# Kernel optimization log

Measured on AMD Instinct MI355X. Metric: run time of the kernel, lower is better.

## Reference

```python
import jax, jax.numpy as jnp
import numpy as np

N = 100000
NEG_SLOPE = 0.2
ALPHA = 0.5


def _glorot(key, shape):
    fan_in, fan_out = shape[0], shape[-1]
    lim = jnp.sqrt(6.0 / (fan_in + fan_out))
    return jax.random.uniform(key, shape, jnp.float32, -lim, lim)


def setup_inputs() -> dict:
    key = jax.random.key(0)
    ks = jax.random.split(key, 16)
    x = jax.random.normal(ks[0], (N, 512), jnp.float32)
    spatial_edge_index = jax.random.randint(ks[1], (2, 800000), 0, N, jnp.int64)
    gene_sim_edge_index = jax.random.randint(ks[2], (2, 800000), 0, N, jnp.int64)
    # spatial GAT params (in=512 -> hid=256)
    W_sp = _glorot(ks[3], (512, 256)); a_src_sp = _glorot(ks[4], (256,)); a_dst_sp = _glorot(ks[5], (256,)); b_sp = jnp.zeros((256,), jnp.float32)
    # gene-sim GAT params
    W_gs = _glorot(ks[6], (512, 256)); a_src_gs = _glorot(ks[7], (256,)); a_dst_gs = _glorot(ks[8], (256,)); b_gs = jnp.zeros((256,), jnp.float32)
    # fusion GAT params (hid=256 -> out=64)
    W_fu = _glorot(ks[9], (256, 64)); a_src_fu = _glorot(ks[10], (64,)); a_dst_fu = _glorot(ks[11], (64,)); b_fu = jnp.zeros((64,), jnp.float32)
    return {"x": x, "spatial_edge_index": spatial_edge_index, "gene_sim_edge_index": gene_sim_edge_index,
            "W_sp": W_sp, "a_src_sp": a_src_sp, "a_dst_sp": a_dst_sp, "b_sp": b_sp,
            "W_gs": W_gs, "a_src_gs": a_src_gs, "a_dst_gs": a_dst_gs, "b_gs": b_gs,
            "W_fu": W_fu, "a_src_fu": a_src_fu, "a_dst_fu": a_dst_fu, "b_fu": b_fu}


def gat_conv(x, edge_index, W, a_src, a_dst, bias):
    """PyG GATConv, heads=1, concat=False, add_self_loops=True."""
    n = x.shape[0]
    h = x @ W  # [N, H]
    loops = jnp.arange(n, dtype=edge_index.dtype)
    src = jnp.concatenate([edge_index[0], loops])  # message source j
    dst = jnp.concatenate([edge_index[1], loops])  # aggregation target i
    e = jax.nn.leaky_relu((h @ a_src)[src] + (h @ a_dst)[dst], NEG_SLOPE)  # [E+N]
    # segment softmax over incoming edges of each dst node
    m = jax.ops.segment_max(e, dst, num_segments=n)
    ex = jnp.exp(e - m[dst])
    denom = jax.ops.segment_sum(ex, dst, num_segments=n)
    coef = ex / denom[dst]
    out = jax.ops.segment_sum(coef[:, None] * h[src], dst, num_segments=n)
    return out + bias


def reference(x, spatial_edge_index, gene_sim_edge_index,
              W_sp, a_src_sp, a_dst_sp, b_sp,
              W_gs, a_src_gs, a_dst_gs, b_gs,
              W_fu, a_src_fu, a_dst_fu, b_fu):
    h_spatial = jax.nn.elu(gat_conv(x, spatial_edge_index, W_sp, a_src_sp, a_dst_sp, b_sp))
    h_gene = jax.nn.elu(gat_conv(x, gene_sim_edge_index, W_gs, a_src_gs, a_dst_gs, b_gs))
    h_fused = ALPHA * h_gene + (1.0 - ALPHA) * h_spatial
    return gat_conv(h_fused, spatial_edge_index, W_fu, a_src_fu, a_dst_fu, b_fu)
```

## Files before the change

kernel.cpp:

```cpp
#include <hip/hip_runtime.h>
#include <math.h>


#define NEG_SLOPE 0.2f

typedef __attribute__((ext_vector_type(8))) short bf16x8;
typedef __attribute__((ext_vector_type(4))) float f32x4;

__device__ __forceinline__ unsigned short f2bf(float f) {
  unsigned int u = __float_as_uint(f);
  u = (u + 0x7FFFu + ((u >> 16) & 1u)) >> 16;
  return (unsigned short)u;
}
__device__ __forceinline__ float bf2f(unsigned short u) {
  return __uint_as_float((unsigned int)u << 16);
}
__device__ __forceinline__ int rl_i(int v, int l) {
  return __builtin_amdgcn_readlane(v, l);
}
__device__ __forceinline__ float rl_f(float v, int l) {
  return __uint_as_float(__builtin_amdgcn_readlane(__float_as_uint(v), l));
}

#define GLOAD16(g, l)                                                   \
  __builtin_amdgcn_global_load_lds(                                     \
      (const __attribute__((address_space(1))) void*)(g),               \
      (__attribute__((address_space(3))) void*)(l), 16, 0, 0)

__global__ __launch_bounds__(256) void wt_bf16_all(const float* __restrict__ W_sp,
                                                   const float* __restrict__ W_gs,
                                                   const float* __restrict__ W_fu,
                                                   unsigned short* __restrict__ wt_sp,
                                                   unsigned short* __restrict__ wt_gs,
                                                   unsigned short* __restrict__ wt_fu) {
  const int i = blockIdx.x * 256 + threadIdx.x;
  if (i < 131072) {
    const int k = i >> 8, n = i & 255;
    wt_sp[n * 512 + k] = f2bf(W_sp[i]);
  } else if (i < 262144) {
    const int j = i - 131072;
    const int k = j >> 8, n = j & 255;
    wt_gs[n * 512 + k] = f2bf(W_gs[j]);
  } else if (i < 278528) {
    const int j = i - 262144;
    const int k = j >> 6, n = j & 63;
    wt_fu[n * 256 + k] = f2bf(W_fu[j]);
  }
}

__global__ __launch_bounds__(256) void hist2(const int* __restrict__ dst_sp,
                                             const int* __restrict__ dst_gs,
                                             int* __restrict__ deg_sp,
                                             int* __restrict__ deg_gs, int E) {
  const int m = blockIdx.x * 256 + threadIdx.x;
  if (m < E) {
    atomicAdd(&deg_sp[dst_sp[m]], 1);
    atomicAdd(&deg_gs[dst_gs[m]], 1);
  }
}

__global__ __launch_bounds__(256) void scan1_2(const int* __restrict__ deg_sp,
                                               const int* __restrict__ deg_gs,
                                               int* __restrict__ rs_sp,
                                               int* __restrict__ rs_gs,
                                               int* __restrict__ parts2, int N) {
  __shared__ int sm[256];
  const int* deg = blockIdx.y ? deg_gs : deg_sp;
  int* rs = blockIdx.y ? rs_gs : rs_sp;
  int* parts = parts2 + blockIdx.y * 512;
  const int i = blockIdx.x * 256 + threadIdx.x;
  const int v = (i < N) ? deg[i] : 0;
  sm[threadIdx.x] = v;
  __syncthreads();
  for (int off = 1; off < 256; off <<= 1) {
    const int x = (threadIdx.x >= off) ? sm[threadIdx.x - off] : 0;
    __syncthreads();
    sm[threadIdx.x] += x;
    __syncthreads();
  }
  if (i < N) rs[i] = sm[threadIdx.x] - v;
  if (threadIdx.x == 255) parts[blockIdx.x] = sm[255];
}

__global__ __launch_bounds__(512) void scan2_2(int* __restrict__ parts2, int nb) {
  __shared__ int sm[512];
  int* parts = parts2 + blockIdx.x * 512;
  const int t = threadIdx.x;
  const int v = (t < nb) ? parts[t] : 0;
  sm[t] = v;
  __syncthreads();
  for (int off = 1; off < 512; off <<= 1) {
    const int x = (t >= off) ? sm[t - off] : 0;
    __syncthreads();
    sm[t] += x;
    __syncthreads();
  }
  if (t < nb) parts[t] = sm[t] - v;
}

__global__ __launch_bounds__(256) void scan3_2(int* __restrict__ rs_sp,
                                               int* __restrict__ rs_gs,
                                               const int* __restrict__ parts2,
                                               int N, int E) {
  int* rs = blockIdx.y ? rs_gs : rs_sp;
  const int* parts = parts2 + blockIdx.y * 512;
  const int i = blockIdx.x * 256 + threadIdx.x;
  if (i < N) rs[i] += parts[blockIdx.x];
  if (i == 0) rs[N] = E;
}

__global__ __launch_bounds__(256) void scatter2(const int* __restrict__ ei_sp,
                                                const int* __restrict__ ei_gs,
                                                const int* __restrict__ rs_sp,
                                                const int* __restrict__ rs_gs,
                                                int* __restrict__ cur_sp,
                                                int* __restrict__ cur_gs,
                                                int* __restrict__ csr_sp,
                                                int* __restrict__ csr_gs, int E) {
  const int m = blockIdx.x * 256 + threadIdx.x;
  if (m >= E) return;
  {
    const int s = ei_sp[m], d = ei_sp[E + m];
    csr_sp[rs_sp[d] + atomicAdd(&cur_sp[d], 1)] = s;
  }
  {
    const int s = ei_gs[m], d = ei_gs[E + m];
    csr_gs[rs_gs[d] + atomicAdd(&cur_gs[d], 1)] = s;
  }
}

__global__ __launch_bounds__(512) void gemm2_fused(const float* __restrict__ x,
                                                   const unsigned short* __restrict__ wsp,
                                                   const unsigned short* __restrict__ wgs,
                                                   unsigned short* __restrict__ hb_sp,
                                                   unsigned short* __restrict__ hb_gs,
                                                   int M) {
  constexpr int BK = 32;
  constexpr int SAP = 40;
  __shared__ unsigned short sA[64 * SAP];
  __shared__ unsigned short sW[2][256 * BK];
  const int tid = threadIdx.x;
  const int w = tid >> 6, l = tid & 63;
  const int bm = blockIdx.x * 64;
  const int arow = tid >> 3;
  const int acol = (tid & 7) * 4;
  int axr = bm + arow;
  axr = axr < M ? axr : M - 1;
  const float* __restrict__ xrow = x + (size_t)axr * 512;

  f32x4 acc[4][4] = {};
  for (int k0 = 0; k0 < 512; k0 += BK) {
    __syncthreads();
    {
      const float4 v = *(const float4*)(xrow + k0 + acol);
      ushort4 o;
      o.x = f2bf(v.x); o.y = f2bf(v.y); o.z = f2bf(v.z); o.w = f2bf(v.w);
      *(ushort4*)&sA[arow * SAP + acol] = o;
    }
#pragma unroll
    for (int c = 0; c < 2; ++c) {
      const int ch = c * 512 + tid;
      const int row = ch >> 2, kp = (ch & 3) * 8;
      const size_t gb = (size_t)row * 1024 + (size_t)(k0 + kp) * 2;
      const size_t lb = (size_t)(c * 512 + (w << 6)) * 16;
      GLOAD16(((const char*)wsp) + gb, ((char*)sW[0]) + lb);
      GLOAD16(((const char*)wgs) + gb, ((char*)sW[1]) + lb);
    }
    __syncthreads();
    bf16x8 af[4], bf[4];
    const unsigned short* __restrict__ sWw = sW[w >> 2];
    const int wc = (w & 3) * 64;
#pragma unroll
    for (int m = 0; m < 4; ++m)
      af[m] = *(const bf16x8*)&sA[(m * 16 + (l & 15)) * SAP + (l >> 4) * 8];
#pragma unroll
    for (int n = 0; n < 4; ++n)
      bf[n] = *(const bf16x8*)&sWw[(wc + n * 16 + (l & 15)) * BK + (l >> 4) * 8];
#pragma unroll
    for (int m = 0; m < 4; ++m)
#pragma unroll
      for (int n = 0; n < 4; ++n)
        acc[m][n] = __builtin_amdgcn_mfma_f32_16x16x32_bf16(af[m], bf[n], acc[m][n], 0, 0, 0);
  }
  unsigned short* __restrict__ outp = (w >> 2) ? hb_gs : hb_sp;
  const int wc = (w & 3) * 64;
#pragma unroll
  for (int m = 0; m < 4; ++m) {
#pragma unroll
    for (int r = 0; r < 4; ++r) {
      const int row = bm + m * 16 + (l >> 4) * 4 + r;
      if (row < M) {
#pragma unroll
        for (int n = 0; n < 4; ++n)
          outp[(size_t)row * 256 + wc + n * 16 + (l & 15)] = f2bf(acc[m][n][r]);
      }
    }
  }
}

template <int BN>
__global__ __launch_bounds__(256) void gemm_bf16_nt(const unsigned short* __restrict__ A,
                                                    const unsigned short* __restrict__ Bt,
                                                    unsigned short* __restrict__ C,
                                                    int M, int Nc, int K) {
  constexpr int BM = 128, BK = 64;
  constexpr int NW = BN / 64;
  constexpr int MW = 4 / NW;
  constexpr int MF = (BM / MW) / 16;
  constexpr int NF = 4;
  constexpr int ACW = (BM * BK * 2 / 1024) / 4;
  constexpr int BCW = (BN * BK * 2 / 1024) / 4;
  __shared__ unsigned short sA[BM * BK];
  __shared__ unsigned short sB[BN * BK];
  const int tid = threadIdx.x;
  const int w = tid >> 6, l = tid & 63;
  const int wr = w / NW, wc = w % NW;
  const int bm = blockIdx.x * BM;
  const int bn = blockIdx.y * BN;
  const int crow = l >> 3;
  const int cbyte = (l & 7) * 16;

  f32x4 acc[MF][NF] = {};
  for (int k0 = 0; k0 < K; k0 += BK) {
    __syncthreads();
#pragma unroll
    for (int c = 0; c < ACW; ++c) {
      const int ch = w * ACW + c;
      int row = bm + ch * 8 + crow;
      row = row < M ? row : M - 1;
      const char* g = (const char*)A + (size_t)row * K * 2 + (size_t)k0 * 2 + cbyte;
      GLOAD16(g, ((char*)sA) + ch * 1024);
    }
#pragma unroll
    for (int c = 0; c < BCW; ++c) {
      const int ch = w * BCW + c;
      const int row = bn + ch * 8 + crow;
      const char* g = (const char*)Bt + (size_t)row * K * 2 + (size_t)k0 * 2 + cbyte;
      GLOAD16(g, ((char*)sB) + ch * 1024);
    }
    __syncthreads();
#pragma unroll
    for (int ks = 0; ks < 2; ++ks) {
      bf16x8 af[MF], bfr[NF];
#pragma unroll
      for (int m = 0; m < MF; ++m) {
        const int r = wr * (BM / MW) + m * 16 + (l & 15);
        af[m] = *(const bf16x8*)&sA[r * BK + ks * 32 + (l >> 4) * 8];
      }
#pragma unroll
      for (int n = 0; n < NF; ++n) {
        const int r = wc * 64 + n * 16 + (l & 15);
        bfr[n] = *(const bf16x8*)&sB[r * BK + ks * 32 + (l >> 4) * 8];
      }
#pragma unroll
      for (int m = 0; m < MF; ++m)
#pragma unroll
        for (int n = 0; n < NF; ++n)
          acc[m][n] = __builtin_amdgcn_mfma_f32_16x16x32_bf16(af[m], bfr[n], acc[m][n], 0, 0, 0);
    }
  }
#pragma unroll
  for (int m = 0; m < MF; ++m) {
#pragma unroll
    for (int r = 0; r < 4; ++r) {
      const int row = bm + wr * (BM / MW) + m * 16 + (l >> 4) * 4 + r;
      if (row < M) {
#pragma unroll
        for (int n = 0; n < NF; ++n)
          C[(size_t)row * Nc + bn + wc * 64 + n * 16 + (l & 15)] = f2bf(acc[m][n][r]);
      }
    }
  }
}

__global__ __launch_bounds__(256) void alpha2_256(const ushort4* __restrict__ hsp,
                                                  const ushort4* __restrict__ hgs,
                                                  const float* __restrict__ av_sp_s,
                                                  const float* __restrict__ av_sp_d,
                                                  const float* __restrict__ av_gs_s,
                                                  const float* __restrict__ av_gs_d,
                                                  float* __restrict__ asrc_sp,
                                                  float* __restrict__ adst_sp,
                                                  float* __restrict__ asrc_gs,
                                                  float* __restrict__ adst_gs, int N) {
  const int wave = (int)((blockIdx.x * (size_t)blockDim.x + threadIdx.x) >> 6);
  const int lane = threadIdx.x & 63;
  if (wave >= N) return;
  const ushort4 h1 = hsp[(size_t)wave * 64 + lane];
  const ushort4 h2 = hgs[(size_t)wave * 64 + lane];
  const float4 s1 = ((const float4*)av_sp_s)[lane];
  const float4 d1 = ((const float4*)av_sp_d)[lane];
  const float4 s2 = ((const float4*)av_gs_s)[lane];
  const float4 d2 = ((const float4*)av_gs_d)[lane];
  const float a0 = bf2f(h1.x), a1 = bf2f(h1.y), a2 = bf2f(h1.z), a3 = bf2f(h1.w);
  const float b0 = bf2f(h2.x), b1 = bf2f(h2.y), b2 = bf2f(h2.z), b3 = bf2f(h2.w);
  float p0 = a0 * s1.x + a1 * s1.y + a2 * s1.z + a3 * s1.w;
  float p1 = a0 * d1.x + a1 * d1.y + a2 * d1.z + a3 * d1.w;
  float p2 = b0 * s2.x + b1 * s2.y + b2 * s2.z + b3 * s2.w;
  float p3 = b0 * d2.x + b1 * d2.y + b2 * d2.z + b3 * d2.w;
#pragma unroll
  for (int off = 32; off; off >>= 1) {
    p0 += __shfl_down(p0, off);
    p1 += __shfl_down(p1, off);
    p2 += __shfl_down(p2, off);
    p3 += __shfl_down(p3, off);
  }
  if (lane == 0) {
    asrc_sp[wave] = p0; adst_sp[wave] = p1;
    asrc_gs[wave] = p2; adst_gs[wave] = p3;
  }
}

__global__ __launch_bounds__(256) void alpha64(const unsigned short* __restrict__ h,
                                               const float* __restrict__ a_src,
                                               const float* __restrict__ a_dst,
                                               float* __restrict__ asrc,
                                               float* __restrict__ adst, int N) {
  const int wave = (int)((blockIdx.x * (size_t)blockDim.x + threadIdx.x) >> 6);
  const int lane = threadIdx.x & 63;
  if (wave >= N) return;
  const float hv = bf2f(h[(size_t)wave * 64 + lane]);
  float ps = hv * a_src[lane];
  float pd = hv * a_dst[lane];
#pragma unroll
  for (int off = 32; off; off >>= 1) {
    ps += __shfl_down(ps, off);
    pd += __shfl_down(pd, off);
  }
  if (lane == 0) { asrc[wave] = ps; adst[wave] = pd; }
}

template <int EPI>
__global__ __launch_bounds__(256) void agg_csr256(const int* __restrict__ rs,
                                                  const int* __restrict__ csr,
                                                  const float* __restrict__ asrc,
                                                  const float* __restrict__ adst,
                                                  const ushort4* __restrict__ h4,
                                                  const float* __restrict__ bias,
                                                  const ushort4* __restrict__ other16,
                                                  ushort4* __restrict__ out16, int N) {
  const int d = (int)((blockIdx.x * (size_t)blockDim.x + threadIdx.x) >> 6);
  const int lane = threadIdx.x & 63;
  if (d >= N) return;
  const float ad = adst[d];

  float e = asrc[d] + ad;
  e = e > 0.f ? e : NEG_SLOPE * e;
  const float wself = expf(e);
  float denl = (lane == 0) ? wself : 0.f;
  const ushort4 hv = h4[(size_t)d * 64 + lane];
  float ax = wself * bf2f(hv.x), ay = wself * bf2f(hv.y),
        az = wself * bf2f(hv.z), aw = wself * bf2f(hv.w);

  const int base = rs[d], mend = rs[d + 1];
  for (int c = base; c < mend; c += 64) {
    const int m = c + lane;
    int s = 0;
    float w = 0.f;
    if (m < mend) {
      s = csr[m];
      float e2 = asrc[s] + ad;
      e2 = e2 > 0.f ? e2 : NEG_SLOPE * e2;
      w = expf(e2);
    }
    denl += w;
    const int cnt = min(64, mend - c);
    int j = 0;
    for (; j + 3 < cnt; j += 4) {
      const int s0 = rl_i(s, j), s1 = rl_i(s, j + 1), s2 = rl_i(s, j + 2), s3 = rl_i(s, j + 3);
      const float w0 = rl_f(w, j), w1 = rl_f(w, j + 1), w2 = rl_f(w, j + 2), w3 = rl_f(w, j + 3);
      const ushort4 a0 = h4[(size_t)s0 * 64 + lane];
      const ushort4 a1 = h4[(size_t)s1 * 64 + lane];
      const ushort4 a2 = h4[(size_t)s2 * 64 + lane];
      const ushort4 a3 = h4[(size_t)s3 * 64 + lane];
      ax += w0 * bf2f(a0.x) + w1 * bf2f(a1.x) + w2 * bf2f(a2.x) + w3 * bf2f(a3.x);
      ay += w0 * bf2f(a0.y) + w1 * bf2f(a1.y) + w2 * bf2f(a2.y) + w3 * bf2f(a3.y);
      az += w0 * bf2f(a0.z) + w1 * bf2f(a1.z) + w2 * bf2f(a2.z) + w3 * bf2f(a3.z);
      aw += w0 * bf2f(a0.w) + w1 * bf2f(a1.w) + w2 * bf2f(a2.w) + w3 * bf2f(a3.w);
    }
    for (; j < cnt; ++j) {
      const int sj = rl_i(s, j);
      const float wj = rl_f(w, j);
      const ushort4 aj = h4[(size_t)sj * 64 + lane];
      ax += wj * bf2f(aj.x);
      ay += wj * bf2f(aj.y);
      az += wj * bf2f(aj.z);
      aw += wj * bf2f(aj.w);
    }
  }
#pragma unroll
  for (int off = 32; off; off >>= 1) denl += __shfl_xor(denl, off);
  const float inv = 1.f / denl;

  const float4 b4 = ((const float4*)bias)[lane];
  float v[4] = {ax * inv + b4.x, ay * inv + b4.y, az * inv + b4.z, aw * inv + b4.w};
#pragma unroll
  for (int j = 0; j < 4; ++j) v[j] = v[j] > 0.f ? v[j] : (expf(v[j]) - 1.f);
  ushort4 pk;
  if (EPI == 2) {
    const ushort4 ov = other16[(size_t)d * 64 + lane];
    pk.x = f2bf(0.5f * v[0] + 0.5f * bf2f(ov.x));
    pk.y = f2bf(0.5f * v[1] + 0.5f * bf2f(ov.y));
    pk.z = f2bf(0.5f * v[2] + 0.5f * bf2f(ov.z));
    pk.w = f2bf(0.5f * v[3] + 0.5f * bf2f(ov.w));
  } else {
    pk.x = f2bf(v[0]); pk.y = f2bf(v[1]); pk.z = f2bf(v[2]); pk.w = f2bf(v[3]);
  }
  out16[(size_t)d * 64 + lane] = pk;
}

__global__ __launch_bounds__(256) void agg_csr64(const int* __restrict__ rs,
                                                 const int* __restrict__ csr,
                                                 const float* __restrict__ asrc,
                                                 const float* __restrict__ adst,
                                                 const unsigned short* __restrict__ h,
                                                 const float* __restrict__ bias,
                                                 float* __restrict__ outb, int N) {
  const int d = (int)((blockIdx.x * (size_t)blockDim.x + threadIdx.x) >> 6);
  const int lane = threadIdx.x & 63;
  if (d >= N) return;
  const float ad = adst[d];

  float e = asrc[d] + ad;
  e = e > 0.f ? e : NEG_SLOPE * e;
  const float wself = expf(e);
  float denl = (lane == 0) ? wself : 0.f;
  float acc = wself * bf2f(h[(size_t)d * 64 + lane]);

  const int base = rs[d], mend = rs[d + 1];
  for (int c = base; c < mend; c += 64) {
    const int m = c + lane;
    int s = 0;
    float w = 0.f;
    if (m < mend) {
      s = csr[m];
      float e2 = asrc[s] + ad;
      e2 = e2 > 0.f ? e2 : NEG_SLOPE * e2;
      w = expf(e2);
    }
    denl += w;
    const int cnt = min(64, mend - c);
    int j = 0;
    for (; j + 3 < cnt; j += 4) {
      const int s0 = rl_i(s, j), s1 = rl_i(s, j + 1), s2 = rl_i(s, j + 2), s3 = rl_i(s, j + 3);
      const float w0 = rl_f(w, j), w1 = rl_f(w, j + 1), w2 = rl_f(w, j + 2), w3 = rl_f(w, j + 3);
      const float a0 = bf2f(h[(size_t)s0 * 64 + lane]);
      const float a1 = bf2f(h[(size_t)s1 * 64 + lane]);
      const float a2 = bf2f(h[(size_t)s2 * 64 + lane]);
      const float a3 = bf2f(h[(size_t)s3 * 64 + lane]);
      acc += w0 * a0 + w1 * a1 + w2 * a2 + w3 * a3;
    }
    for (; j < cnt; ++j) {
      const int sj = rl_i(s, j);
      const float wj = rl_f(w, j);
      acc += wj * bf2f(h[(size_t)sj * 64 + lane]);
    }
  }
#pragma unroll
  for (int off = 32; off; off >>= 1) denl += __shfl_xor(denl, off);
  outb[(size_t)d * 64 + lane] = acc / denl + bias[lane];
}

extern "C" void kernel_launch(void* const* d_in, const int* in_sizes, int n_in,
                              void* d_out, int out_size, void* d_ws, size_t ws_size,
                              hipStream_t stream) {
  const float* x        = (const float*)d_in[0];
  const int*   ei_sp    = (const int*)d_in[1];
  const int*   ei_gs    = (const int*)d_in[2];
  const float* W_sp     = (const float*)d_in[3];
  const float* a_src_sp = (const float*)d_in[4];
  const float* a_dst_sp = (const float*)d_in[5];
  const float* b_sp     = (const float*)d_in[6];
  const float* W_gs     = (const float*)d_in[7];
  const float* a_src_gs = (const float*)d_in[8];
  const float* a_dst_gs = (const float*)d_in[9];
  const float* b_gs     = (const float*)d_in[10];
  const float* W_fu     = (const float*)d_in[11];
  const float* a_src_fu = (const float*)d_in[12];
  const float* a_dst_fu = (const float*)d_in[13];
  const float* b_fu     = (const float*)d_in[14];
  float* out = (float*)d_out;

  const int N = in_sizes[0] / 512;
  const int E = in_sizes[1] / 2;
  const int nb = (N + 255) / 256;

  unsigned short* wt_sp = (unsigned short*)d_ws;
  unsigned short* wt_gs = wt_sp + 256 * 512;
  unsigned short* wt_fu = wt_gs + 256 * 512;
  unsigned short* hb_sp = wt_fu + 64 * 256;
  unsigned short* hb_gs = hb_sp + (size_t)N * 256;
  unsigned short* B3    = hb_gs + (size_t)N * 256;
  unsigned short* hfb   = B3 + (size_t)N * 256;
  float* asrc_sp = (float*)(hfb + (size_t)N * 256);
  float* adst_sp = asrc_sp + N;
  float* asrc_gs = adst_sp + N;
  float* adst_gs = asrc_gs + N;
  int* rs_sp  = (int*)(adst_gs + N);
  int* rs_gs  = rs_sp + (N + 1);
  int* csr_sp = rs_gs + (N + 1);
  int* csr_gs = csr_sp + E;
  int* deg_sp = csr_gs + E;
  int* deg_gs = deg_sp + N;
  int* parts2 = deg_gs + N;

  unsigned short* hfu = B3;

  const int BLK = 256;
  const int eGrid = (E + BLK - 1) / BLK;
  const int nodeWaveGrid = (N + 3) / 4;
  const dim3 gFu((N + 127) / 128, 1);

  hipMemsetAsync(deg_sp, 0, (size_t)2 * N * 4, stream);
  hist2<<<eGrid, BLK, 0, stream>>>(ei_sp + E, ei_gs + E, deg_sp, deg_gs, E);
  scan1_2<<<dim3(nb, 2), BLK, 0, stream>>>(deg_sp, deg_gs, rs_sp, rs_gs, parts2, N);
  scan2_2<<<2, 512, 0, stream>>>(parts2, nb);
  scan3_2<<<dim3(nb, 2), BLK, 0, stream>>>(rs_sp, rs_gs, parts2, N, E);
  hipMemsetAsync(deg_sp, 0, (size_t)2 * N * 4, stream);
  scatter2<<<eGrid, BLK, 0, stream>>>(ei_sp, ei_gs, rs_sp, rs_gs, deg_sp, deg_gs,
                                      csr_sp, csr_gs, E);

  wt_bf16_all<<<(278528 + 255) / 256, BLK, 0, stream>>>(W_sp, W_gs, W_fu,
                                                        wt_sp, wt_gs, wt_fu);

  gemm2_fused<<<(N + 63) / 64, 512, 0, stream>>>(x, wt_sp, wt_gs, hb_sp, hb_gs, N);

  alpha2_256<<<nodeWaveGrid, BLK, 0, stream>>>((const ushort4*)hb_sp,
                                               (const ushort4*)hb_gs,
                                               a_src_sp, a_dst_sp, a_src_gs, a_dst_gs,
                                               asrc_sp, adst_sp, asrc_gs, adst_gs, N);

  agg_csr256<1><<<nodeWaveGrid, BLK, 0, stream>>>(rs_sp, csr_sp, asrc_sp, adst_sp,
                                                  (const ushort4*)hb_sp, b_sp,
                                                  nullptr, (ushort4*)B3, N);

  agg_csr256<2><<<nodeWaveGrid, BLK, 0, stream>>>(rs_gs, csr_gs, asrc_gs, adst_gs,
                                                  (const ushort4*)hb_gs, b_gs,
                                                  (const ushort4*)B3, (ushort4*)hfb, N);

  gemm_bf16_nt<64><<<gFu, BLK, 0, stream>>>(hfb, wt_fu, hfu, N, 64, 256);
  alpha64<<<nodeWaveGrid, BLK, 0, stream>>>(hfu, a_src_fu, a_dst_fu,
                                            asrc_sp, adst_sp, N);
  agg_csr64<<<nodeWaveGrid, BLK, 0, stream>>>(rs_sp, csr_sp, asrc_sp, adst_sp,
                                              hfu, b_fu, out, N);
}
```

Measured before the change: 563.2 us.

## Double K-tile to 64 and XOR-swizzle LDS layout in fused dual GEMM

The fused spatial/gene-sim projection GEMM now uses a K tile of 64 instead of 32. That halves the number of barrier-separated iterations and gives each iteration two MFMA k-steps. The shared-memory layout for both the activation tile and the weight tiles is XOR-swizzled to avoid bank conflicts, which replaces padding. Each half of the block now loads only its own weight matrix. The cost is more LDS per block (about 72KB), which may reduce occupancy.

```diff
diff --git a/kernel.cpp b/kernel.cpp
--- a/kernel.cpp
+++ b/kernel.cpp
@@ -135,55 +135,64 @@
                                                    unsigned short* __restrict__ hb_sp,
                                                    unsigned short* __restrict__ hb_gs,
                                                    int M) {
-  constexpr int BK = 32;
-  constexpr int SAP = 40;
-  __shared__ unsigned short sA[64 * SAP];
-  __shared__ unsigned short sW[2][256 * BK];
+  __shared__ unsigned short sA[64 * 64];
+  __shared__ unsigned short sW[2][256 * 64];
   const int tid = threadIdx.x;
   const int w = tid >> 6, l = tid & 63;
+  const int whalf = w >> 2;
+  const int wq = w & 3;
   const int bm = blockIdx.x * 64;
-  const int arow = tid >> 3;
-  const int acol = (tid & 7) * 4;
-  int axr = bm + arow;
-  axr = axr < M ? axr : M - 1;
-  const float* __restrict__ xrow = x + (size_t)axr * 512;
+
+  const int arow0 = tid >> 4;
+  const int acol4 = (tid & 15) * 4;
+  const unsigned short* __restrict__ wtp = whalf ? wgs : wsp;
+  const int wrow_in_ch = l >> 3;
+  const int wbyte = ((l & 7) * 16) ^ ((wrow_in_ch & 7) << 4);
 
   f32x4 acc[4][4] = {};
-  for (int k0 = 0; k0 < 512; k0 += BK) {
-    __syncthreads();
-    {
-      const float4 v = *(const float4*)(xrow + k0 + acol);
+  for (int k0 = 0; k0 < 512; k0 += 64) {
+    __syncthreads();
+#pragma unroll
+    for (int r = 0; r < 2; ++r) {
+      const int row = arow0 + r * 32;
+      int grow = bm + row;
+      grow = grow < M ? grow : M - 1;
+      const float4 v = *(const float4*)(x + (size_t)grow * 512 + k0 + acol4);
       ushort4 o;
       o.x = f2bf(v.x); o.y = f2bf(v.y); o.z = f2bf(v.z); o.w = f2bf(v.w);
-      *(ushort4*)&sA[arow * SAP + acol] = o;
-    }
-#pragma unroll
-    for (int c = 0; c < 2; ++c) {
-      const int ch = c * 512 + tid;
-      const int row = ch >> 2, kp = (ch & 3) * 8;
-      const size_t gb = (size_t)row * 1024 + (size_t)(k0 + kp) * 2;
-      const size_t lb = (size_t)(c * 512 + (w << 6)) * 16;
-      GLOAD16(((const char*)wsp) + gb, ((char*)sW[0]) + lb);
-      GLOAD16(((const char*)wgs) + gb, ((char*)sW[1]) + lb);
-    }
-    __syncthreads();
-    bf16x8 af[4], bf[4];
-    const unsigned short* __restrict__ sWw = sW[w >> 2];
-    const int wc = (w & 3) * 64;
-#pragma unroll
-    for (int m = 0; m < 4; ++m)
-      af[m] = *(const bf16x8*)&sA[(m * 16 + (l & 15)) * SAP + (l >> 4) * 8];
-#pragma unroll
-    for (int n = 0; n < 4; ++n)
-      bf[n] = *(const bf16x8*)&sWw[(wc + n * 16 + (l & 15)) * BK + (l >> 4) * 8];
-#pragma unroll
-    for (int m = 0; m < 4; ++m)
-#pragma unroll
-      for (int n = 0; n < 4; ++n)
-        acc[m][n] = __builtin_amdgcn_mfma_f32_16x16x32_bf16(af[m], bf[n], acc[m][n], 0, 0, 0);
-  }
-  unsigned short* __restrict__ outp = (w >> 2) ? hb_gs : hb_sp;
-  const int wc = (w & 3) * 64;
+      const int byte = (row * 128 + acol4 * 2) ^ ((row & 7) << 4);
+      *(ushort4*)(((char*)sA) + byte) = o;
+    }
+#pragma unroll
+    for (int c = 0; c < 8; ++c) {
+      const int ch = c * 4 + wq;
+      const int grow = ch * 8 + wrow_in_ch;
+      const char* g = (const char*)wtp + (size_t)grow * 1024 + (size_t)k0 * 2 + wbyte;
+      GLOAD16(g, ((char*)sW[whalf]) + ch * 1024);
+    }
+    __syncthreads();
+#pragma unroll
+    for (int ks = 0; ks < 2; ++ks) {
+      const int cb = ks * 64 + (l >> 4) * 16;
+      bf16x8 af[4], bf[4];
+#pragma unroll
+      for (int m = 0; m < 4; ++m) {
+        const int r = m * 16 + (l & 15);
+        af[m] = *(const bf16x8*)(((const char*)sA) + r * 128 + (cb ^ ((r & 7) << 4)));
+      }
+#pragma unroll
+      for (int n = 0; n < 4; ++n) {
+        const int r = wq * 64 + n * 16 + (l & 15);
+        bf[n] = *(const bf16x8*)(((const char*)sW[whalf]) + r * 128 + (cb ^ ((r & 7) << 4)));
+      }
+#pragma unroll
+      for (int m = 0; m < 4; ++m)
+#pragma unroll
+        for (int n = 0; n < 4; ++n)
+          acc[m][n] = __builtin_amdgcn_mfma_f32_16x16x32_bf16(af[m], bf[n], acc[m][n], 0, 0, 0);
+    }
+  }
+  unsigned short* __restrict__ outp = whalf ? hb_gs : hb_sp;
 #pragma unroll
   for (int m = 0; m < 4; ++m) {
 #pragma unroll
@@ -192,7 +201,7 @@
       if (row < M) {
 #pragma unroll
         for (int n = 0; n < 4; ++n)
-          outp[(size_t)row * 256 + wc + n * 16 + (l & 15)] = f2bf(acc[m][n][r]);
+          outp[(size_t)row * 256 + wq * 64 + n * 16 + (l & 15)] = f2bf(acc[m][n][r]);
       }
     }
   }
```

New measurement: 527.3 us. 6.4% less time.
